# Optimization experiments

Measured on AMD Instinct MI355X. Metric: run time of the kernel, lower is better.

## Reference

```python
import jax, jax.numpy as jnp
from jax import lax
import numpy as np

# ---- constants mirroring args ----
T = 8192          # signal length
NUM_CH = 64       # eeg channels
LSTM_SIZE = 256
NUM_CLS = 40
NUM_PROP = 1024   # candidate proposals before NMS
NUM_PROP_AFTER = 256
PROP_LEN = 128    # extracted window length
IOU_THRESH = 0.5


def setup_inputs() -> dict:
    key = jax.random.key(0)
    ks = jax.random.split(key, 12)
    data = jax.random.normal(ks[0], (T, NUM_CH), dtype=jnp.float32)
    # proposals: (start, end, score), 1-D temporal intervals
    starts = jax.random.uniform(ks[1], (NUM_PROP,), minval=0.0, maxval=float(T - PROP_LEN))
    lens = jax.random.uniform(ks[2], (NUM_PROP,), minval=32.0, maxval=float(PROP_LEN))
    scores = jax.random.uniform(ks[3], (NUM_PROP,))
    proposals = jnp.stack([starts, starts + lens, scores], axis=-1).astype(jnp.float32)

    H, C = LSTM_SIZE, NUM_CH
    s_ih = 1.0 / np.sqrt(C)
    s_hh = 1.0 / np.sqrt(H)
    W_ih = jax.random.uniform(ks[4], (4 * H, C), minval=-s_ih, maxval=s_ih)
    W_hh = jax.random.uniform(ks[5], (4 * H, H), minval=-s_hh, maxval=s_hh)
    b_ih = jax.random.uniform(ks[6], (4 * H,), minval=-s_hh, maxval=s_hh)
    b_hh = jax.random.uniform(ks[7], (4 * H,), minval=-s_hh, maxval=s_hh)
    s_h = 1.0 / np.sqrt(H)
    W_cls = jax.random.uniform(ks[8], (NUM_CLS, H), minval=-s_h, maxval=s_h)
    b_cls = jax.random.uniform(ks[9], (NUM_CLS,), minval=-s_h, maxval=s_h)
    W_bbox = jax.random.uniform(ks[10], (2 * NUM_CLS, H), minval=-s_h, maxval=s_h)
    b_bbox = jax.random.uniform(ks[11], (2 * NUM_CLS,), minval=-s_h, maxval=s_h)
    return {"data": data, "proposals": proposals, "W_ih": W_ih, "W_hh": W_hh,
            "b_ih": b_ih, "b_hh": b_hh, "W_cls": W_cls, "b_cls": b_cls,
            "W_bbox": W_bbox, "b_bbox": b_bbox}


def _nms_1d(starts, ends, scores, iou_thresh):
    """Greedy 1-D interval NMS. Returns indices (into original order) of the
    first NUM_PROP_AFTER surviving proposals, in descending-score order."""
    order = jnp.argsort(-scores)
    s, e = starts[order], ends[order]
    n = s.shape[0]
    idx = jnp.arange(n)

    def body(i, sup):
        inter = jnp.maximum(0.0, jnp.minimum(e[i], e) - jnp.maximum(s[i], s))
        union = (e[i] - s[i]) + (e - s) - inter
        iou = inter / jnp.maximum(union, 1e-6)
        new = sup | ((iou > iou_thresh) & (idx > i) & (~sup[i]))
        return new

    suppressed = lax.fori_loop(0, n, body, jnp.zeros(n, dtype=bool))
    keep = ~suppressed
    # stable sort: kept proposals first, preserving score order
    sel = jnp.argsort(jnp.where(keep, 0, 1), stable=True)[:NUM_PROP_AFTER]
    return order[sel]


def _lstm_last(x, W_ih, W_hh, b_ih, b_hh):
    """x: [K, L, C]; returns last hidden state [K, H] (torch gate order ifgo)."""
    K = x.shape[0]
    H = W_hh.shape[1]
    h0 = jnp.zeros((K, H), x.dtype)
    c0 = jnp.zeros((K, H), x.dtype)
    b = b_ih + b_hh

    def step(carry, xt):
        h, c = carry
        gates = xt @ W_ih.T + h @ W_hh.T + b  # [K, 4H]
        i, f, g, o = jnp.split(gates, 4, axis=-1)
        i = jax.nn.sigmoid(i)
        f = jax.nn.sigmoid(f)
        g = jnp.tanh(g)
        o = jax.nn.sigmoid(o)
        c = f * c + i * g
        h = o * jnp.tanh(c)
        return (h, c), None

    (h, _), _ = lax.scan(step, (h0, c0), jnp.swapaxes(x, 0, 1))
    return h


def reference(data, proposals, W_ih, W_hh, b_ih, b_hh, W_cls, b_cls, W_bbox, b_bbox):
    starts, ends, scores = proposals[:, 0], proposals[:, 1], proposals[:, 2]
    # NMS + truncate to num_prop_after (training branch of original)
    kept = _nms_1d(starts, ends, scores, IOU_THRESH)            # [K]
    # extract fixed-length eeg windows at proposal starts (gather)
    t0 = jnp.clip(jnp.round(starts[kept]).astype(jnp.int32), 0, T - PROP_LEN)
    win_idx = t0[:, None] + jnp.arange(PROP_LEN)[None, :]       # [K, L]
    eeg_proposals = data[win_idx]                               # [K, L, C]
    # region LSTM -> last timestep feature
    base_feat = _lstm_last(eeg_proposals, W_ih, W_hh, b_ih, b_hh)  # [K, H]
    cls_feat = base_feat @ W_cls.T + b_cls                      # [K, num_cls]
    bbox_feat = base_feat @ W_bbox.T + b_bbox                   # [K, 2*num_cls]
    return cls_feat, bbox_feat
```

## Files before the change

kernel.cpp:

```cpp
#include <hip/hip_runtime.h>
#include <math.h>

#define T_LEN 8192
#define NUM_CH 64
#define HID 256
#define NUM_CLS 40
#define NUM_PROP 1024
#define NUM_PROP_AFTER 256
#define PROP_LEN 128

#define MS 4
#define NGRP 64
#define NSL 4
#define KH 320
#define KSEGN 4
#define SEGH 80
#define HXPAR 65536

typedef _Float16 h2_t __attribute__((ext_vector_type(2)));
union U32H2 { unsigned int u; h2_t h; };
union HU16 { _Float16 h; unsigned short u; };

#if defined(__has_builtin)
#if __has_builtin(__builtin_amdgcn_fdot2)
#define HAS_FDOT2 1
#endif
#endif

__device__ __forceinline__ float dot2f(unsigned int wa, unsigned int hb, float acc) {
    U32H2 a, b;
    a.u = wa;
    b.u = hb;
#ifdef HAS_FDOT2
    return __builtin_amdgcn_fdot2(a.h, b.h, acc, false);
#else
    return acc + (float)a.h[0] * (float)b.h[0] + (float)a.h[1] * (float)b.h[1];
#endif
}

__device__ __forceinline__ float dot8f(const uint4& w, const uint4& h, float acc) {
    acc = dot2f(w.x, h.x, acc);
    acc = dot2f(w.y, h.y, acc);
    acc = dot2f(w.z, h.z, acc);
    acc = dot2f(w.w, h.w, acc);
    return acc;
}

__device__ __forceinline__ float fsigmoid(float x) { return 1.0f / (1.0f + __expf(-x)); }
__device__ __forceinline__ float ftanh(float x) {
    float e = __expf(-2.0f * fabsf(x));
    float t = (1.0f - e) / (1.0f + e);
    return copysignf(t, x);
}

__device__ __forceinline__ unsigned int pack2(float a, float b) {
    HU16 ha, hb;
    ha.h = (_Float16)a;
    hb.h = (_Float16)b;
    return (unsigned int)ha.u | ((unsigned int)hb.u << 16);
}

__global__ __launch_bounds__(1024, 4) void fused_kernel(
    const float* __restrict__ data, const float* __restrict__ prop,
    const float* __restrict__ W_ih, const float* __restrict__ W_hh,
    const float* __restrict__ b_ih, const float* __restrict__ b_hh,
    const float* __restrict__ W_cls, const float* __restrict__ b_cls,
    const float* __restrict__ W_bbox, const float* __restrict__ b_bbox,
    float* __restrict__ out, unsigned int* __restrict__ t0s,
    unsigned int* __restrict__ Hx32) {
    __shared__ __align__(16) _Float16 hx[MS][KH];
    __shared__ __align__(16) float pp[MS][KSEGN][256];

    const int tid = threadIdx.x;
    const int g = blockIdx.x & (NGRP - 1);
    const int s = blockIdx.x >> 6;
    const int kseg = tid >> 8;
    const int rl = tid & 255;

    if (blockIdx.x == 0) {
        float* sc_p = &pp[0][0][0];
        float* ss = &pp[1][0][0];
        float* se = &pp[2][0][0];
        unsigned char* sup = (unsigned char*)&pp[3][0][0];
        unsigned long long* cmask =
            (unsigned long long*)((char*)&pp[3][0][0] + 1024);

        float ps = prop[tid * 3 + 0];
        float pe = prop[tid * 3 + 1];
        float pc = prop[tid * 3 + 2];
        sc_p[tid] = pc;
        sup[tid] = 0;
        __syncthreads();

        int r = 0;
        for (int j = 0; j < NUM_PROP; ++j) {
            float o = sc_p[j];
            r += (o > pc) || (o == pc && j < tid);
        }
        ss[r] = ps;
        se[r] = pe;
        __syncthreads();

        const float my_s = ss[tid];
        const float my_e = se[tid];
        const float my_len = my_e - my_s;
        bool mysup = false;

        for (int ci = 0; ci < 16; ++ci) {
            if (tid < 64) {
                int i = ci * 64 + tid;
                float is_ = ss[i], ie_ = se[i];
                unsigned long long m = __ballot(sup[i] != 0);
                for (int l = 0; l < 64; ++l) {
                    if (!((m >> l) & 1)) {
                        float ls = __shfl(is_, l);
                        float le = __shfl(ie_, l);
                        float inter = fmaxf(fminf(le, ie_) - fmaxf(ls, is_), 0.0f);
                        float uni = (le - ls) + (ie_ - is_) - inter;
                        float iou = inter / fmaxf(uni, 1e-6f);
                        unsigned long long nb = __ballot((tid > l) && (iou > 0.5f));
                        m |= nb;
                    }
                }
                sup[i] = (unsigned char)((m >> tid) & 1);
                if (tid == 0) cmask[ci] = ~m;
            }
            __syncthreads();
            unsigned long long am = cmask[ci];
            for (int l = 0; l < 64; ++l) {
                if ((am >> l) & 1) {
                    int i = ci * 64 + l;
                    if (tid > i && !mysup) {
                        float ls = ss[i], le = se[i];
                        float inter = fmaxf(fminf(le, my_e) - fmaxf(ls, my_s), 0.0f);
                        float uni = (le - ls) + my_len - inter;
                        if (inter / fmaxf(uni, 1e-6f) > 0.5f) mysup = true;
                    }
                }
            }
            sup[tid] = mysup ? 1 : 0;
            __syncthreads();
        }

        int myc = tid >> 6;
        unsigned long long mybit = 1ull << (tid & 63);
        int kb = 0, kt = 0;
        for (int c2 = 0; c2 < 16; ++c2) {
            int p = __popcll(cmask[c2]);
            kt += p;
            if (c2 < myc) kb += p;
        }
        kb += __popcll(cmask[myc] & (mybit - 1));
        int slot = (cmask[myc] & mybit) ? kb : (kt + (tid - kb));
        if (slot < NUM_PROP_AFTER) {
            int t0v = (int)rintf(my_s);
            t0v = max(0, min(t0v, T_LEN - PROP_LEN));
            __hip_atomic_store(&t0s[slot], (unsigned int)t0v | 0x80000000u,
                               __ATOMIC_RELAXED, __HIP_MEMORY_SCOPE_AGENT);
        }
        asm volatile("s_waitcnt vmcnt(0)" ::: "memory");
        __syncthreads();
    }

    uint4 Wr[10];
    {
        const int gate = rl >> 6, unit = rl & 63;
        const int grow = gate * 256 + s * 64 + unit;
        const float* __restrict__ baseh = W_hh + grow * HID;
        const float* __restrict__ basex = W_ih + grow * NUM_CH;
#pragma unroll
        for (int j = 0; j < 10; ++j) {
            const int kh = kseg * SEGH + j * 8;
            const float* src = (kh < 256) ? (baseh + kh) : (basex + (kh - 256));
            float4 f0 = *(const float4*)(src);
            float4 f1 = *(const float4*)(src + 4);
            Wr[j] = make_uint4(pack2(f0.x, f0.y), pack2(f0.z, f0.w),
                               pack2(f1.x, f1.y), pack2(f1.z, f1.w));
        }
    }

    const int aq = tid >> 6;
    const int au = tid & 63;
    float bi = 0.f, bf = 0.f, bg = 0.f, bo = 0.f, c_st = 0.f;
    int xt0 = 0;
    if (tid < 256) {
        int u = s * 64 + au;
        bi = b_ih[u] + b_hh[u];
        bf = b_ih[256 + u] + b_hh[256 + u];
        bg = b_ih[512 + u] + b_hh[512 + u];
        bo = b_ih[768 + u] + b_hh[768 + u];
    }

    const int li = tid - 256;
    const int gp = li >> 7;
    const int rem = li & 127;
    const int gsq2 = rem >> 5;
    const int gu2 = (rem & 31) * 2;
    const int sp2 = gp + (gp >= s ? 1 : 0);
    const int goff = (g * MS + gsq2) * HID + sp2 * 64 + gu2;

    hx[tid >> 8][tid & 255] = (_Float16)0.0f;

    if (tid < 256) {
        const unsigned int* tp = &t0s[g * MS + aq];
        unsigned int tv;
        for (;;) {
            tv = __hip_atomic_load(tp, __ATOMIC_RELAXED, __HIP_MEMORY_SCOPE_AGENT);
            if (tv & 0x80000000u) break;
            __builtin_amdgcn_s_sleep(8);
        }
        xt0 = (int)(tv & 0x7FFFFFFFu);
        hx[aq][256 + au] = (_Float16)data[xt0 * NUM_CH + au];
    }
    __syncthreads();

    for (int t = 0; t < PROP_LEN; ++t) {
        float xnext = 0.0f;
        if (tid < 256 && t + 1 < PROP_LEN)
            xnext = data[(xt0 + t + 1) * NUM_CH + au];

        float a0 = 0.f, a1 = 0.f, a2 = 0.f, a3 = 0.f;
#pragma unroll
        for (int j = 0; j < 10; ++j) {
            const int hb = kseg * SEGH + j * 8;
            uint4 h0 = *(const uint4*)&hx[0][hb];
            uint4 h1 = *(const uint4*)&hx[1][hb];
            uint4 h2 = *(const uint4*)&hx[2][hb];
            uint4 h3 = *(const uint4*)&hx[3][hb];
            uint4 w = Wr[j];
            a0 = dot8f(w, h0, a0);
            a1 = dot8f(w, h1, a1);
            a2 = dot8f(w, h2, a2);
            a3 = dot8f(w, h3, a3);
        }
        pp[0][kseg][rl] = a0;
        pp[1][kseg][rl] = a1;
        pp[2][kseg][rl] = a2;
        pp[3][kseg][rl] = a3;
        __syncthreads();

        const unsigned int tagv = (unsigned int)(t + 1);
        const int par = (t + 1) & 1;
        if (tid < 256) {
            float si = pp[aq][0][au] + pp[aq][1][au] + pp[aq][2][au] +
                       pp[aq][3][au] + bi;
            float sf = pp[aq][0][64 + au] + pp[aq][1][64 + au] +
                       pp[aq][2][64 + au] + pp[aq][3][64 + au] + bf;
            float sg = pp[aq][0][128 + au] + pp[aq][1][128 + au] +
                       pp[aq][2][128 + au] + pp[aq][3][128 + au] + bg;
            float so = pp[aq][0][192 + au] + pp[aq][1][192 + au] +
                       pp[aq][2][192 + au] + pp[aq][3][192 + au] + bo;
            float gi = fsigmoid(si), gf = fsigmoid(sf);
            float gg = ftanh(sg), go = fsigmoid(so);
            c_st = gf * c_st + gi * gg;
            float h = go * ftanh(c_st);
            HU16 hu;
            hu.h = (_Float16)h;
            unsigned int myw = (tagv << 16) | (unsigned int)hu.u;
            unsigned int pw = __shfl_xor(myw, 1);
            if ((au & 1) == 0) {
                unsigned long long dw =
                    (unsigned long long)myw | ((unsigned long long)pw << 32);
                __hip_atomic_store(
                    (unsigned long long*)&Hx32[par * HXPAR +
                                               (g * MS + aq) * HID + s * 64 + au],
                    dw, __ATOMIC_RELAXED, __HIP_MEMORY_SCOPE_AGENT);
            }
            hx[aq][s * 64 + au] = hu.h;
            if (t + 1 < PROP_LEN) hx[aq][256 + au] = (_Float16)xnext;
        } else if (tid < 640) {
            const unsigned long long* ga =
                (const unsigned long long*)(Hx32 + par * HXPAR + goff);
            unsigned long long v =
                __hip_atomic_load(ga, __ATOMIC_RELAXED, __HIP_MEMORY_SCOPE_AGENT);
            while (__builtin_expect(((unsigned int)v >> 16) != tagv ||
                                        ((unsigned int)(v >> 32) >> 16) != tagv,
                                    0)) {
                __builtin_amdgcn_s_sleep(1);
                v = __hip_atomic_load(ga, __ATOMIC_RELAXED,
                                      __HIP_MEMORY_SCOPE_AGENT);
            }
            unsigned int lo = (unsigned int)v;
            unsigned int hi = (unsigned int)(v >> 32);
            unsigned int packed = (lo & 0xFFFFu) | (hi << 16);
            *(unsigned int*)&hx[gsq2][sp2 * 64 + gu2] = packed;
        }
        __syncthreads();
    }

    if (tid < MS * 30) {
        int sq = tid / 30;
        int ml = tid % 30;
        int m = s * 30 + ml;
        const float* Wrow;
        float acc;
        int oidx;
        if (m < NUM_CLS) {
            Wrow = W_cls + m * HID;
            acc = b_cls[m];
            oidx = (g * MS + sq) * NUM_CLS + m;
        } else {
            int mb = m - NUM_CLS;
            Wrow = W_bbox + mb * HID;
            acc = b_bbox[mb];
            oidx = NUM_PROP_AFTER * NUM_CLS + (g * MS + sq) * 2 * NUM_CLS + mb;
        }
        const float4* w4 = (const float4*)Wrow;
        const _Float16* hp = &hx[sq][0];
        for (int c = 0; c < 32; ++c) {
            float4 wa = w4[c * 2 + 0];
            float4 wb = w4[c * 2 + 1];
            acc += (float)hp[c * 8 + 0] * wa.x + (float)hp[c * 8 + 1] * wa.y +
                   (float)hp[c * 8 + 2] * wa.z + (float)hp[c * 8 + 3] * wa.w +
                   (float)hp[c * 8 + 4] * wb.x + (float)hp[c * 8 + 5] * wb.y +
                   (float)hp[c * 8 + 6] * wb.z + (float)hp[c * 8 + 7] * wb.w;
        }
        out[oidx] = acc;
    }
}

extern "C" void kernel_launch(void* const* d_in, const int* in_sizes, int n_in,
                              void* d_out, int out_size, void* d_ws,
                              size_t ws_size, hipStream_t stream) {
    const float* data = (const float*)d_in[0];
    const float* prop = (const float*)d_in[1];
    const float* W_ih = (const float*)d_in[2];
    const float* W_hh = (const float*)d_in[3];
    const float* b_ih = (const float*)d_in[4];
    const float* b_hh = (const float*)d_in[5];
    const float* W_cls = (const float*)d_in[6];
    const float* b_cls = (const float*)d_in[7];
    const float* W_bbox = (const float*)d_in[8];
    const float* b_bbox = (const float*)d_in[9];
    float* out = (float*)d_out;

    unsigned int* t0s = (unsigned int*)d_ws;
    unsigned int* Hx32 = (unsigned int*)((char*)d_ws + 4096);

    hipMemsetAsync(d_ws, 0, 4096 + 2 * HXPAR * 4, stream);

    void* kargs[] = {(void*)&data,  (void*)&prop,   (void*)&W_ih,  (void*)&W_hh,
                     (void*)&b_ih,  (void*)&b_hh,   (void*)&W_cls, (void*)&b_cls,
                     (void*)&W_bbox, (void*)&b_bbox, (void*)&out,  (void*)&t0s,
                     (void*)&Hx32};
    hipLaunchCooperativeKernel((void*)fused_kernel, dim3(NSL * NGRP), dim3(1024),
                               kargs, 0, stream);
}
```

Before: 642.5 us.

## Reorder hidden-state layout so local h and x are consumed before remote h arrives

Moves each block's own hidden slice and the input x to the front of the shared hx vector, with remote slices behind them. The matching weights are permuted so that kseg 0 and part of kseg 1 can start their dot products before the cross-block hidden values arrive. The remote fetch now runs at the start of the next step on 384 threads and signals per-wave LDS flags, which replaces waiting on a full barrier. The cost is extra spin-waiting on shared flags and more complex indexing in the final projection. Remote h for the last step is fetched separately after the loop.

```diff
diff --git a/kernel.cpp b/kernel.cpp
--- a/kernel.cpp
+++ b/kernel.cpp
@@ -70,6 +70,7 @@
     unsigned int* __restrict__ Hx32) {
     __shared__ __align__(16) _Float16 hx[MS][KH];
     __shared__ __align__(16) float pp[MS][KSEGN][256];
+    __shared__ volatile unsigned int gfl[6];
 
     const int tid = threadIdx.x;
     const int g = blockIdx.x & (NGRP - 1);
@@ -166,13 +167,22 @@
     {
         const int gate = rl >> 6, unit = rl & 63;
         const int grow = gate * 256 + s * 64 + unit;
-        const float* __restrict__ baseh = W_hh + grow * HID;
-        const float* __restrict__ basex = W_ih + grow * NUM_CH;
+        const float* __restrict__ bh = W_hh + grow * HID;
+        const float* __restrict__ bx = W_ih + grow * NUM_CH;
 #pragma unroll
         for (int j = 0; j < 10; ++j) {
-            const int kh = kseg * SEGH + j * 8;
-            const float* src = (kh < 256) ? (baseh + kh) : (basex + (kh - 256));
-            float4 f0 = *(const float4*)(src);
+            const int kp = kseg * SEGH + j * 8;
+            const float* src;
+            if (kp < 64) {
+                src = bh + s * 64 + kp;
+            } else if (kp < 128) {
+                src = bx + (kp - 64);
+            } else {
+                int q = (kp - 128) >> 6, v = (kp - 128) & 63;
+                int sp = q + (q >= s ? 1 : 0);
+                src = bh + sp * 64 + v;
+            }
+            float4 f0 = *(const float4*)src;
             float4 f1 = *(const float4*)(src + 4);
             Wr[j] = make_uint4(pack2(f0.x, f0.y), pack2(f0.z, f0.w),
                                pack2(f1.x, f1.y), pack2(f1.z, f1.w));
@@ -191,15 +201,18 @@
         bo = b_ih[768 + u] + b_hh[768 + u];
     }
 
-    const int li = tid - 256;
-    const int gp = li >> 7;
+    const int li = tid - 512;
+    const int q_ = li >> 7;
     const int rem = li & 127;
-    const int gsq2 = rem >> 5;
+    const int gsq = rem >> 5;
     const int gu2 = (rem & 31) * 2;
-    const int sp2 = gp + (gp >= s ? 1 : 0);
-    const int goff = (g * MS + gsq2) * HID + sp2 * 64 + gu2;
-
-    hx[tid >> 8][tid & 255] = (_Float16)0.0f;
+    const int sp_ = q_ + (q_ >= s ? 1 : 0);
+    const int goff = (g * MS + gsq) * HID + sp_ * 64 + gu2;
+    const int gw = (tid >> 6) - 8;
+
+    ((unsigned short*)hx)[tid] = 0;
+    if (tid < 256) ((unsigned short*)hx)[1024 + tid] = 0;
+    if (tid < 6) gfl[tid] = 0;
 
     if (tid < 256) {
         const unsigned int* tp = &t0s[g * MS + aq];
@@ -210,7 +223,7 @@
             __builtin_amdgcn_s_sleep(8);
         }
         xt0 = (int)(tv & 0x7FFFFFFFu);
-        hx[aq][256 + au] = (_Float16)data[xt0 * NUM_CH + au];
+        hx[aq][64 + au] = (_Float16)data[xt0 * NUM_CH + au];
     }
     __syncthreads();
 
@@ -220,19 +233,67 @@
             xnext = data[(xt0 + t + 1) * NUM_CH + au];
 
         float a0 = 0.f, a1 = 0.f, a2 = 0.f, a3 = 0.f;
-#pragma unroll
-        for (int j = 0; j < 10; ++j) {
-            const int hb = kseg * SEGH + j * 8;
-            uint4 h0 = *(const uint4*)&hx[0][hb];
-            uint4 h1 = *(const uint4*)&hx[1][hb];
-            uint4 h2 = *(const uint4*)&hx[2][hb];
-            uint4 h3 = *(const uint4*)&hx[3][hb];
-            uint4 w = Wr[j];
-            a0 = dot8f(w, h0, a0);
-            a1 = dot8f(w, h1, a1);
-            a2 = dot8f(w, h2, a2);
-            a3 = dot8f(w, h3, a3);
-        }
+#define DOTJ(J)                                                         \
+        {                                                               \
+            const int hb = kseg * SEGH + (J) * 8;                       \
+            uint4 h0 = *(const uint4*)&hx[0][hb];                       \
+            uint4 h1 = *(const uint4*)&hx[1][hb];                       \
+            uint4 h2 = *(const uint4*)&hx[2][hb];                       \
+            uint4 h3 = *(const uint4*)&hx[3][hb];                       \
+            uint4 w = Wr[(J)];                                          \
+            a0 = dot8f(w, h0, a0);                                      \
+            a1 = dot8f(w, h1, a1);                                      \
+            a2 = dot8f(w, h2, a2);                                      \
+            a3 = dot8f(w, h3, a3);                                      \
+        }
+
+        if (kseg == 0) {
+            DOTJ(0) DOTJ(1) DOTJ(2) DOTJ(3) DOTJ(4)
+            DOTJ(5) DOTJ(6) DOTJ(7) DOTJ(8) DOTJ(9)
+        } else if (kseg == 1) {
+            DOTJ(0) DOTJ(1) DOTJ(2) DOTJ(3) DOTJ(4) DOTJ(5)
+        }
+
+        if (t >= 1 && tid >= 512 && tid < 896) {
+            const unsigned int tagv = (unsigned int)t;
+            const int par = t & 1;
+            const unsigned long long* ga =
+                (const unsigned long long*)(Hx32 + par * HXPAR + goff);
+            unsigned long long v =
+                __hip_atomic_load(ga, __ATOMIC_RELAXED, __HIP_MEMORY_SCOPE_AGENT);
+            while (__builtin_expect(((unsigned int)v >> 16) != tagv ||
+                                        ((unsigned int)(v >> 32) >> 16) != tagv,
+                                    0)) {
+                __builtin_amdgcn_s_sleep(2);
+                v = __hip_atomic_load(ga, __ATOMIC_RELAXED,
+                                      __HIP_MEMORY_SCOPE_AGENT);
+            }
+            unsigned int lo = (unsigned int)v;
+            unsigned int hi = (unsigned int)(v >> 32);
+            *(unsigned int*)&hx[gsq][128 + q_ * 64 + gu2] =
+                (lo & 0xFFFFu) | (hi << 16);
+            asm volatile("s_waitcnt lgkmcnt(0)" ::: "memory");
+            if ((tid & 63) == 0) gfl[gw] = (unsigned int)t;
+        }
+
+        if (kseg != 0) {
+            if (t >= 1) {
+                while (gfl[0] < (unsigned int)t || gfl[1] < (unsigned int)t ||
+                       gfl[2] < (unsigned int)t || gfl[3] < (unsigned int)t ||
+                       gfl[4] < (unsigned int)t || gfl[5] < (unsigned int)t) {
+                    __builtin_amdgcn_s_sleep(1);
+                }
+                asm volatile("" ::: "memory");
+            }
+            if (kseg == 1) {
+                DOTJ(6) DOTJ(7) DOTJ(8) DOTJ(9)
+            } else {
+                DOTJ(0) DOTJ(1) DOTJ(2) DOTJ(3) DOTJ(4)
+                DOTJ(5) DOTJ(6) DOTJ(7) DOTJ(8) DOTJ(9)
+            }
+        }
+#undef DOTJ
+
         pp[0][kseg][rl] = a0;
         pp[1][kseg][rl] = a1;
         pp[2][kseg][rl] = a2;
@@ -266,27 +327,27 @@
                                                (g * MS + aq) * HID + s * 64 + au],
                     dw, __ATOMIC_RELAXED, __HIP_MEMORY_SCOPE_AGENT);
             }
-            hx[aq][s * 64 + au] = hu.h;
-            if (t + 1 < PROP_LEN) hx[aq][256 + au] = (_Float16)xnext;
-        } else if (tid < 640) {
-            const unsigned long long* ga =
-                (const unsigned long long*)(Hx32 + par * HXPAR + goff);
-            unsigned long long v =
-                __hip_atomic_load(ga, __ATOMIC_RELAXED, __HIP_MEMORY_SCOPE_AGENT);
-            while (__builtin_expect(((unsigned int)v >> 16) != tagv ||
-                                        ((unsigned int)(v >> 32) >> 16) != tagv,
-                                    0)) {
-                __builtin_amdgcn_s_sleep(1);
-                v = __hip_atomic_load(ga, __ATOMIC_RELAXED,
-                                      __HIP_MEMORY_SCOPE_AGENT);
-            }
-            unsigned int lo = (unsigned int)v;
-            unsigned int hi = (unsigned int)(v >> 32);
-            unsigned int packed = (lo & 0xFFFFu) | (hi << 16);
-            *(unsigned int*)&hx[gsq2][sp2 * 64 + gu2] = packed;
+            hx[aq][au] = hu.h;
+            if (t + 1 < PROP_LEN) hx[aq][64 + au] = (_Float16)xnext;
         }
         __syncthreads();
     }
+
+    if (tid >= 512 && tid < 896) {
+        const unsigned int tagv = (unsigned int)PROP_LEN;
+        const unsigned long long* ga = (const unsigned long long*)(Hx32 + goff);
+        unsigned long long v =
+            __hip_atomic_load(ga, __ATOMIC_RELAXED, __HIP_MEMORY_SCOPE_AGENT);
+        while (((unsigned int)v >> 16) != tagv ||
+               ((unsigned int)(v >> 32) >> 16) != tagv) {
+            __builtin_amdgcn_s_sleep(2);
+            v = __hip_atomic_load(ga, __ATOMIC_RELAXED, __HIP_MEMORY_SCOPE_AGENT);
+        }
+        unsigned int lo = (unsigned int)v;
+        unsigned int hi = (unsigned int)(v >> 32);
+        *(unsigned int*)&hx[gsq][128 + q_ * 64 + gu2] = (lo & 0xFFFFu) | (hi << 16);
+    }
+    __syncthreads();
 
     if (tid < MS * 30) {
         int sq = tid / 30;
@@ -305,15 +366,13 @@
             acc = b_bbox[mb];
             oidx = NUM_PROP_AFTER * NUM_CLS + (g * MS + sq) * 2 * NUM_CLS + mb;
         }
-        const float4* w4 = (const float4*)Wrow;
         const _Float16* hp = &hx[sq][0];
-        for (int c = 0; c < 32; ++c) {
-            float4 wa = w4[c * 2 + 0];
-            float4 wb = w4[c * 2 + 1];
-            acc += (float)hp[c * 8 + 0] * wa.x + (float)hp[c * 8 + 1] * wa.y +
-                   (float)hp[c * 8 + 2] * wa.z + (float)hp[c * 8 + 3] * wa.w +
-                   (float)hp[c * 8 + 4] * wb.x + (float)hp[c * 8 + 5] * wb.y +
-                   (float)hp[c * 8 + 6] * wb.z + (float)hp[c * 8 + 7] * wb.w;
+        for (int k = 0; k < 64; ++k) acc += Wrow[s * 64 + k] * (float)hp[k];
+        for (int q2 = 0; q2 < 3; ++q2) {
+            int sp2 = q2 + (q2 >= s ? 1 : 0);
+            const float* wr = Wrow + sp2 * 64;
+            const _Float16* hr = hp + 128 + q2 * 64;
+            for (int v2 = 0; v2 < 64; ++v2) acc += wr[v2] * (float)hr[v2];
         }
         out[oidx] = acc;
     }
```

New measurement: 628.2 us (median of 3 runs). 1.02x faster.
